# Performance work log

Hardware: AMD Instinct MI355X
Metric: run time of the kernel (lower is better)

Reference implementation:

```python
import jax, jax.numpy as jnp
import numpy as np

EMBED_DIM = 1024
NUM_HEADS = 16
HEAD_DIM = EMBED_DIM // NUM_HEADS
B, S = 2, 2048


def setup_inputs() -> dict:
    key = jax.random.key(0)
    ks = jax.random.split(key, 9)
    scale = 1.0 / np.sqrt(EMBED_DIM)
    return {
        "x": jax.random.normal(ks[0], (B, S, EMBED_DIM), dtype=jnp.float32),
        "Wq": jax.random.normal(ks[1], (EMBED_DIM, EMBED_DIM), dtype=jnp.float32) * scale,
        "bq": jnp.zeros((EMBED_DIM,), dtype=jnp.float32),
        "Wk": jax.random.normal(ks[2], (EMBED_DIM, EMBED_DIM), dtype=jnp.float32) * scale,
        "bk": jnp.zeros((EMBED_DIM,), dtype=jnp.float32),
        "Wv": jax.random.normal(ks[3], (EMBED_DIM, EMBED_DIM), dtype=jnp.float32) * scale,
        "bv": jnp.zeros((EMBED_DIM,), dtype=jnp.float32),
        "Wo": jax.random.normal(ks[4], (EMBED_DIM, EMBED_DIM), dtype=jnp.float32) * scale,
        "bo": jnp.zeros((EMBED_DIM,), dtype=jnp.float32),
    }


def _split_heads(t):
    # [B, S, E] -> [B, H, S, Dh]
    b, s, _ = t.shape
    return t.reshape(b, s, NUM_HEADS, HEAD_DIM).transpose(0, 2, 1, 3)


def reference(x, Wq, bq, Wk, bk, Wv, bv, Wo, bo):
    q = _split_heads(x @ Wq + bq)
    k = _split_heads(x @ Wk + bk)
    v = _split_heads(x @ Wv + bv)
    scale = jnp.sqrt(jnp.asarray(HEAD_DIM, dtype=x.dtype))
    scores = jnp.einsum("bhqd,bhkd->bhqk", q, k) / scale
    attn = jax.nn.softmax(scores, axis=-1)
    out = jnp.einsum("bhqk,bhkd->bhqd", attn, v)  # [B,H,S,Dh]
    out = out.transpose(0, 2, 1, 3).reshape(x.shape[0], x.shape[1], EMBED_DIM)
    return out @ Wo + bo
```

## Files before the change

### kernel.cpp

```cpp
#include <hip/hip_runtime.h>
#include <math.h>
#include <stdint.h>

typedef __bf16 bf16;
typedef __bf16 bf16x4 __attribute__((ext_vector_type(4)));
typedef __bf16 bf16x8 __attribute__((ext_vector_type(8)));
typedef float f32x4 __attribute__((ext_vector_type(4)));

constexpr int E = 1024;
constexpr int S = 2048;
constexpr int H = 16;

__device__ __forceinline__ void gload16(const void* g, void* l) {
  __builtin_amdgcn_global_load_lds(
      (__attribute__((address_space(1))) void*)(uintptr_t)g,
      (__attribute__((address_space(3))) void*)(uint32_t)(uintptr_t)l, 16, 0, 0);
}

__device__ __forceinline__ f32x4 mfma16(bf16x8 a, bf16x8 b, f32x4 c) {
  return __builtin_amdgcn_mfma_f32_16x16x32_bf16(a, b, c, 0, 0, 0);
}

__global__ __launch_bounds__(256) void cast_x(const float* __restrict__ x,
                                              bf16* __restrict__ o) {
  const size_t i = ((size_t)blockIdx.x * 256 + threadIdx.x) * 8;
  const float4 a = *(const float4*)(x + i);
  const float4 b = *(const float4*)(x + i + 4);
  bf16x8 r;
  r[0] = (bf16)a.x; r[1] = (bf16)a.y; r[2] = (bf16)a.z; r[3] = (bf16)a.w;
  r[4] = (bf16)b.x; r[5] = (bf16)b.y; r[6] = (bf16)b.z; r[7] = (bf16)b.w;
  *(bf16x8*)(o + i) = r;
}

__global__ __launch_bounds__(256) void transpose_cast_w(
    const float* __restrict__ W0, const float* __restrict__ W1,
    const float* __restrict__ W2, const float* __restrict__ W3,
    bf16* __restrict__ T0, bf16* __restrict__ T1, bf16* __restrict__ T2,
    bf16* __restrict__ T3) {
  const float* W;
  bf16* T;
  switch (blockIdx.z) {
    case 0: W = W0; T = T0; break;
    case 1: W = W1; T = T1; break;
    case 2: W = W2; T = T2; break;
    default: W = W3; T = T3; break;
  }
  __shared__ float t[64][65];
  const int k0 = blockIdx.y * 64, n0 = blockIdx.x * 64;
  const int tr = threadIdx.x >> 4;
  const int tc = (threadIdx.x & 15) * 4;
#pragma unroll
  for (int u = 0; u < 4; ++u) {
    const float4 v = *(const float4*)(W + (size_t)(k0 + tr + u * 16) * E + n0 + tc);
    t[tr + u * 16][tc + 0] = v.x;
    t[tr + u * 16][tc + 1] = v.y;
    t[tr + u * 16][tc + 2] = v.z;
    t[tr + u * 16][tc + 3] = v.w;
  }
  __syncthreads();
#pragma unroll
  for (int u = 0; u < 4; ++u) {
    const int n = tr + u * 16;
    bf16x4 o;
#pragma unroll
    for (int i = 0; i < 4; ++i) o[i] = (bf16)t[tc + i][n];
    *(bf16x4*)(T + (size_t)(n0 + n) * E + k0 + tc) = o;
  }
}

__global__ __launch_bounds__(256) void gemm_qkv(const bf16* __restrict__ A,
                                                const bf16* __restrict__ Wt,
                                                const float* __restrict__ bq,
                                                const float* __restrict__ bk,
                                                const float* __restrict__ bv,
                                                bf16* __restrict__ qo,
                                                bf16* __restrict__ ko,
                                                bf16* __restrict__ vo) {
  __shared__ __attribute__((aligned(16))) bf16 Asm[128 * 32];
  __shared__ __attribute__((aligned(16))) bf16 Bsm[128 * 32];
  const int z = blockIdx.z;
  const bf16* Bt = Wt + (size_t)z * E * E;
  const float* bias = (z == 0) ? bq : (z == 1) ? bk : bv;
  const int tid = threadIdx.x;
  const int w = tid >> 6, lane = tid & 63, quad = lane >> 4, ln = lane & 15;
  const int bm = blockIdx.y * 128, bn = blockIdx.x * 128;
  const int wr = w >> 1, wc = w & 1;
  const int srow = w * 32 + (lane >> 2);
  const int scol = (lane & 3) * 8;
  const bf16* Ag = A + (size_t)(bm + srow) * E + scol;
  const bf16* Bg = Bt + (size_t)(bn + srow) * E + scol;
  f32x4 acc[4][4] = {};

  for (int k0 = 0; k0 < E; k0 += 32) {
    gload16(Ag + k0, &Asm[(w * 32) * 32]);
    gload16(Ag + k0 + (size_t)16 * E, &Asm[(w * 32 + 16) * 32]);
    gload16(Bg + k0, &Bsm[(w * 32) * 32]);
    gload16(Bg + k0 + (size_t)16 * E, &Bsm[(w * 32 + 16) * 32]);
    __syncthreads();
    bf16x8 af[4], bfr[4];
#pragma unroll
    for (int t = 0; t < 4; ++t) {
      af[t] = *(const bf16x8*)&Asm[(wr * 64 + t * 16 + ln) * 32 + quad * 8];
      bfr[t] = *(const bf16x8*)&Bsm[(wc * 64 + t * 16 + ln) * 32 + quad * 8];
    }
#pragma unroll
    for (int rt = 0; rt < 4; ++rt)
#pragma unroll
      for (int ct = 0; ct < 4; ++ct)
        acc[rt][ct] = mfma16(af[rt], bfr[ct], acc[rt][ct]);
    __syncthreads();
  }

  const float scl = (z == 0) ? 0.125f : 1.0f;
  float bvv[4];
#pragma unroll
  for (int ct = 0; ct < 4; ++ct) bvv[ct] = bias[bn + wc * 64 + ct * 16 + ln];
#pragma unroll
  for (int rt = 0; rt < 4; ++rt) {
    const int row0 = bm + wr * 64 + rt * 16 + quad * 4;
#pragma unroll
    for (int ct = 0; ct < 4; ++ct) {
      const int c = bn + wc * 64 + ct * 16 + ln;
      if (z == 2) {
        bf16x4 p;
#pragma unroll
        for (int r = 0; r < 4; ++r) p[r] = (bf16)(acc[rt][ct][r] + bvv[ct]);
        const int bb = row0 >> 11;
        const int sin = row0 & 2047;
        *(bf16x4*)&vo[((size_t)(bb << 10) + c) * S + sin] = p;
      } else {
        bf16* o = (z == 0) ? qo : ko;
#pragma unroll
        for (int r = 0; r < 4; ++r)
          o[(size_t)(row0 + r) * E + c] = (bf16)((acc[rt][ct][r] + bvv[ct]) * scl);
      }
    }
  }
}

__global__ __launch_bounds__(256) void gemm_wo(const bf16* __restrict__ A,
                                               const bf16* __restrict__ Bt,
                                               const float* __restrict__ bias,
                                               float* __restrict__ C) {
  __shared__ __attribute__((aligned(16))) bf16 Asm[64 * 32];
  __shared__ __attribute__((aligned(16))) bf16 Bsm[128 * 32];
  const int tid = threadIdx.x;
  const int w = tid >> 6, lane = tid & 63, quad = lane >> 4, ln = lane & 15;
  const int bm = blockIdx.y * 64, bn = blockIdx.x * 128;
  const int wr = w >> 1, wc = w & 1;
  const int sr = lane >> 2, sc = (lane & 3) * 8;
  const bf16* Ag = A + (size_t)(bm + w * 16 + sr) * E + sc;
  const bf16* Bg = Bt + (size_t)(bn + w * 32 + sr) * E + sc;
  f32x4 acc[2][4] = {};

  for (int k0 = 0; k0 < E; k0 += 32) {
    gload16(Ag + k0, &Asm[(w * 16) * 32]);
    gload16(Bg + k0, &Bsm[(w * 32) * 32]);
    gload16(Bg + k0 + (size_t)16 * E, &Bsm[(w * 32 + 16) * 32]);
    __syncthreads();
    bf16x8 af[2], bfr[4];
#pragma unroll
    for (int t = 0; t < 2; ++t)
      af[t] = *(const bf16x8*)&Asm[(wr * 32 + t * 16 + ln) * 32 + quad * 8];
#pragma unroll
    for (int t = 0; t < 4; ++t)
      bfr[t] = *(const bf16x8*)&Bsm[(wc * 64 + t * 16 + ln) * 32 + quad * 8];
#pragma unroll
    for (int rt = 0; rt < 2; ++rt)
#pragma unroll
      for (int ct = 0; ct < 4; ++ct)
        acc[rt][ct] = mfma16(af[rt], bfr[ct], acc[rt][ct]);
    __syncthreads();
  }

  float bvv[4];
#pragma unroll
  for (int ct = 0; ct < 4; ++ct) bvv[ct] = bias[bn + wc * 64 + ct * 16 + ln];
#pragma unroll
  for (int rt = 0; rt < 2; ++rt) {
    const int row0 = bm + wr * 32 + rt * 16 + quad * 4;
#pragma unroll
    for (int ct = 0; ct < 4; ++ct) {
      const int c = bn + wc * 64 + ct * 16 + ln;
#pragma unroll
      for (int r = 0; r < 4; ++r)
        C[(size_t)(row0 + r) * E + c] = acc[rt][ct][r] + bvv[ct];
    }
  }
}

__global__ __launch_bounds__(256) void attn_mfma(const bf16* __restrict__ Qg,
                                                 const bf16* __restrict__ Kg,
                                                 const bf16* __restrict__ Vt,
                                                 bf16* __restrict__ Og) {
  __shared__ __attribute__((aligned(16))) bf16 Qs[2][64][32];
  __shared__ __attribute__((aligned(16))) bf16 Ks[2][2][64][32];
  __shared__ __attribute__((aligned(16))) bf16 Vs[2][2][64][32];
  __shared__ __attribute__((aligned(16))) bf16 Pl[4][16][72];
  const int tid = threadIdx.x;
  const int w = tid >> 6, lane = tid & 63, quad = lane >> 4, ln = lane & 15;
  const int q0 = blockIdx.x * 64, h = blockIdx.y, b = blockIdx.z;
  const size_t qkb = ((size_t)b * S) * E + (size_t)h * 64;
  const size_t vtb = ((size_t)b * E + (size_t)h * 64) * S;
  const int sr = lane >> 2, sc = (lane & 3) * 8;

#pragma unroll
  for (int hf = 0; hf < 2; ++hf)
    gload16(Qg + qkb + (size_t)(q0 + w * 16 + sr) * E + hf * 32 + sc,
            &Qs[hf][w * 16][0]);

  const bf16* Kp = Kg + qkb + (size_t)(w * 16 + sr) * E + sc;
  const bf16* Vp = Vt + vtb + (size_t)(w * 16 + sr) * S + sc;

  bf16x8 kr[2], vr[2];
#pragma unroll
  for (int hf = 0; hf < 2; ++hf) {
    kr[hf] = *(const bf16x8*)(Kp + hf * 32);
    vr[hf] = *(const bf16x8*)(Vp + hf * 32);
  }
#pragma unroll
  for (int hf = 0; hf < 2; ++hf) {
    *(bf16x8*)&Ks[0][hf][w * 16 + sr][sc] = kr[hf];
    *(bf16x8*)&Vs[0][hf][w * 16 + sr][sc] = vr[hf];
  }

  float lpart[4] = {};
  f32x4 oacc[4] = {};
  bf16x8 qf[2];
  int cur = 0;

  for (int kt = 0; kt < S; kt += 64) {
    __syncthreads();
    const bool more = (kt + 64 < S);
    if (more) {
#pragma unroll
      for (int hf = 0; hf < 2; ++hf) {
        kr[hf] = *(const bf16x8*)(Kp + (size_t)(kt + 64) * E + hf * 32);
        vr[hf] = *(const bf16x8*)(Vp + (kt + 64) + hf * 32);
      }
    }
    if (kt == 0) {
#pragma unroll
      for (int hf = 0; hf < 2; ++hf)
        qf[hf] = *(const bf16x8*)&Qs[hf][w * 16 + ln][quad * 8];
    }

    f32x4 sc4[4];
#pragma unroll
    for (int ct = 0; ct < 4; ++ct) {
      f32x4 z = {};
      z = mfma16(qf[0], *(const bf16x8*)&Ks[cur][0][ct * 16 + ln][quad * 8], z);
      z = mfma16(qf[1], *(const bf16x8*)&Ks[cur][1][ct * 16 + ln][quad * 8], z);
      sc4[ct] = z;
    }

#pragma unroll
    for (int r = 0; r < 4; ++r) {
#pragma unroll
      for (int ct = 0; ct < 4; ++ct) {
        const float p = __expf(sc4[ct][r]);
        lpart[r] += p;
        Pl[w][quad * 4 + r][ct * 16 + ln] = (bf16)p;
      }
    }
    asm volatile("s_waitcnt lgkmcnt(0)" ::: "memory");
    const bf16x8 pf0 = *(const bf16x8*)&Pl[w][ln][quad * 8];
    const bf16x8 pf1 = *(const bf16x8*)&Pl[w][ln][32 + quad * 8];
#pragma unroll
    for (int ct = 0; ct < 4; ++ct) {
      oacc[ct] = mfma16(pf0, *(const bf16x8*)&Vs[cur][0][ct * 16 + ln][quad * 8],
                        oacc[ct]);
      oacc[ct] = mfma16(pf1, *(const bf16x8*)&Vs[cur][1][ct * 16 + ln][quad * 8],
                        oacc[ct]);
    }

    if (more) {
#pragma unroll
      for (int hf = 0; hf < 2; ++hf) {
        *(bf16x8*)&Ks[cur ^ 1][hf][w * 16 + sr][sc] = kr[hf];
        *(bf16x8*)&Vs[cur ^ 1][hf][w * 16 + sr][sc] = vr[hf];
      }
    }
    cur ^= 1;
  }

#pragma unroll
  for (int r = 0; r < 4; ++r) {
#pragma unroll
    for (int off = 1; off < 16; off <<= 1) lpart[r] += __shfl_xor(lpart[r], off);
  }
  float inv[4];
#pragma unroll
  for (int r = 0; r < 4; ++r) inv[r] = 1.0f / lpart[r];
#pragma unroll
  for (int ct = 0; ct < 4; ++ct) {
#pragma unroll
    for (int r = 0; r < 4; ++r) {
      Og[qkb + (size_t)(q0 + w * 16 + quad * 4 + r) * E + ct * 16 + ln] =
          (bf16)(oacc[ct][r] * inv[r]);
    }
  }
}

extern "C" void kernel_launch(void* const* d_in, const int* in_sizes, int n_in,
                              void* d_out, int out_size, void* d_ws, size_t ws_size,
                              hipStream_t stream) {
  const float* x = (const float*)d_in[0];
  const float* Wq = (const float*)d_in[1];
  const float* bq = (const float*)d_in[2];
  const float* Wk = (const float*)d_in[3];
  const float* bk = (const float*)d_in[4];
  const float* Wv = (const float*)d_in[5];
  const float* bv = (const float*)d_in[6];
  const float* Wo = (const float*)d_in[7];
  const float* bo = (const float*)d_in[8];

  const size_t ME = (size_t)4096 * 1024;
  const size_t WE = (size_t)1024 * 1024;
  bf16* xb = (bf16*)d_ws;
  bf16* wqt = xb + ME;
  bf16* wkt = wqt + WE;
  bf16* wvt = wkt + WE;
  bf16* wot = wvt + WE;
  bf16* qb = wot + WE;
  bf16* kb = qb + ME;
  bf16* vt = kb + ME;
  bf16* ab = vt + ME;

  cast_x<<<2048, 256, 0, stream>>>(x, xb);
  transpose_cast_w<<<dim3(16, 16, 4), 256, 0, stream>>>(Wq, Wk, Wv, Wo, wqt, wkt,
                                                        wvt, wot);
  gemm_qkv<<<dim3(8, 32, 3), 256, 0, stream>>>(xb, wqt, bq, bk, bv, qb, kb, vt);
  attn_mfma<<<dim3(32, 16, 2), 256, 0, stream>>>(qb, kb, vt, ab);
  gemm_wo<<<dim3(8, 64), 256, 0, stream>>>(ab, wot, bo, (float*)d_out);
}
```

Before: 209.6 us.

## Use 32x32 MFMA tiles with 128 queries per attention block

Rewrites the attention kernel to use 32x32x16 bf16 MFMA, with each wave handling 32 query rows and computing transposed scores so softmax outputs map directly to row-per-lane layout. Each block now covers 128 queries, doubling reuse of every K/V tile loaded into shared memory and halving the grid. Q is held in registers, loaded directly from global memory, and the LDS tiles are padded. The trade-off is fewer blocks for the GPU's CUs and higher register pressure from the 16-wide accumulators.

```diff
diff --git a/kernel.cpp b/kernel.cpp
--- a/kernel.cpp
+++ b/kernel.cpp
@@ -6,6 +6,7 @@
 typedef __bf16 bf16x4 __attribute__((ext_vector_type(4)));
 typedef __bf16 bf16x8 __attribute__((ext_vector_type(8)));
 typedef float f32x4 __attribute__((ext_vector_type(4)));
+typedef float f32x16 __attribute__((ext_vector_type(16)));
 
 constexpr int E = 1024;
 constexpr int S = 2048;
@@ -19,6 +20,9 @@
 
 __device__ __forceinline__ f32x4 mfma16(bf16x8 a, bf16x8 b, f32x4 c) {
   return __builtin_amdgcn_mfma_f32_16x16x32_bf16(a, b, c, 0, 0, 0);
+}
+__device__ __forceinline__ f32x16 mfma32(bf16x8 a, bf16x8 b, f32x16 c) {
+  return __builtin_amdgcn_mfma_f32_32x32x16_bf16(a, b, c, 0, 0, 0);
 }
 
 __global__ __launch_bounds__(256) void cast_x(const float* __restrict__ x,
@@ -193,111 +197,113 @@
                                                  const bf16* __restrict__ Kg,
                                                  const bf16* __restrict__ Vt,
                                                  bf16* __restrict__ Og) {
-  __shared__ __attribute__((aligned(16))) bf16 Qs[2][64][32];
-  __shared__ __attribute__((aligned(16))) bf16 Ks[2][2][64][32];
-  __shared__ __attribute__((aligned(16))) bf16 Vs[2][2][64][32];
-  __shared__ __attribute__((aligned(16))) bf16 Pl[4][16][72];
+  __shared__ __attribute__((aligned(16))) bf16 Ks[2][64][72];
+  __shared__ __attribute__((aligned(16))) bf16 Vs[2][64][72];
+  __shared__ __attribute__((aligned(16))) bf16 Pl[4][32][72];
   const int tid = threadIdx.x;
-  const int w = tid >> 6, lane = tid & 63, quad = lane >> 4, ln = lane & 15;
-  const int q0 = blockIdx.x * 64, h = blockIdx.y, b = blockIdx.z;
+  const int w = tid >> 6, lane = tid & 63, ln = lane & 31, hf = lane >> 5;
+  const int q0 = blockIdx.x * 128, h = blockIdx.y, b = blockIdx.z;
   const size_t qkb = ((size_t)b * S) * E + (size_t)h * 64;
   const size_t vtb = ((size_t)b * E + (size_t)h * 64) * S;
-  const int sr = lane >> 2, sc = (lane & 3) * 8;
-
-#pragma unroll
-  for (int hf = 0; hf < 2; ++hf)
-    gload16(Qg + qkb + (size_t)(q0 + w * 16 + sr) * E + hf * 32 + sc,
-            &Qs[hf][w * 16][0]);
-
-  const bf16* Kp = Kg + qkb + (size_t)(w * 16 + sr) * E + sc;
-  const bf16* Vp = Vt + vtb + (size_t)(w * 16 + sr) * S + sc;
+  const int sr = tid >> 2;
+  const int sc = (tid & 3) * 16;
+
+  bf16x8 qf[4];
+  {
+    const bf16* qrow = Qg + qkb + (size_t)(q0 + w * 32 + ln) * E + hf * 8;
+#pragma unroll
+    for (int c = 0; c < 4; ++c) qf[c] = *(const bf16x8*)(qrow + 16 * c);
+  }
+
+  const bf16* Kp = Kg + qkb + (size_t)sr * E + sc;
+  const bf16* Vp = Vt + vtb + (size_t)sr * S + sc;
 
   bf16x8 kr[2], vr[2];
-#pragma unroll
-  for (int hf = 0; hf < 2; ++hf) {
-    kr[hf] = *(const bf16x8*)(Kp + hf * 32);
-    vr[hf] = *(const bf16x8*)(Vp + hf * 32);
-  }
-#pragma unroll
-  for (int hf = 0; hf < 2; ++hf) {
-    *(bf16x8*)&Ks[0][hf][w * 16 + sr][sc] = kr[hf];
-    *(bf16x8*)&Vs[0][hf][w * 16 + sr][sc] = vr[hf];
-  }
-
-  float lpart[4] = {};
-  f32x4 oacc[4] = {};
-  bf16x8 qf[2];
+  kr[0] = *(const bf16x8*)(Kp);
+  kr[1] = *(const bf16x8*)(Kp + 8);
+  vr[0] = *(const bf16x8*)(Vp);
+  vr[1] = *(const bf16x8*)(Vp + 8);
+  *(bf16x8*)&Ks[0][sr][sc] = kr[0];
+  *(bf16x8*)&Ks[0][sr][sc + 8] = kr[1];
+  *(bf16x8*)&Vs[0][sr][sc] = vr[0];
+  *(bf16x8*)&Vs[0][sr][sc + 8] = vr[1];
+
+  float lpart = 0.f;
+  f32x16 oacc[2] = {};
   int cur = 0;
 
   for (int kt = 0; kt < S; kt += 64) {
     __syncthreads();
     const bool more = (kt + 64 < S);
     if (more) {
-#pragma unroll
-      for (int hf = 0; hf < 2; ++hf) {
-        kr[hf] = *(const bf16x8*)(Kp + (size_t)(kt + 64) * E + hf * 32);
-        vr[hf] = *(const bf16x8*)(Vp + (kt + 64) + hf * 32);
+      kr[0] = *(const bf16x8*)(Kp + (size_t)(kt + 64) * E);
+      kr[1] = *(const bf16x8*)(Kp + (size_t)(kt + 64) * E + 8);
+      vr[0] = *(const bf16x8*)(Vp + (kt + 64));
+      vr[1] = *(const bf16x8*)(Vp + (kt + 64) + 8);
+    }
+
+    f32x16 st[2] = {};
+#pragma unroll
+    for (int mt = 0; mt < 2; ++mt) {
+#pragma unroll
+      for (int c = 0; c < 4; ++c) {
+        const bf16x8 ka =
+            *(const bf16x8*)&Ks[cur][mt * 32 + ln][c * 16 + hf * 8];
+        st[mt] = mfma32(ka, qf[c], st[mt]);
       }
     }
-    if (kt == 0) {
-#pragma unroll
-      for (int hf = 0; hf < 2; ++hf)
-        qf[hf] = *(const bf16x8*)&Qs[hf][w * 16 + ln][quad * 8];
-    }
-
-    f32x4 sc4[4];
-#pragma unroll
-    for (int ct = 0; ct < 4; ++ct) {
-      f32x4 z = {};
-      z = mfma16(qf[0], *(const bf16x8*)&Ks[cur][0][ct * 16 + ln][quad * 8], z);
-      z = mfma16(qf[1], *(const bf16x8*)&Ks[cur][1][ct * 16 + ln][quad * 8], z);
-      sc4[ct] = z;
-    }
-
-#pragma unroll
-    for (int r = 0; r < 4; ++r) {
-#pragma unroll
-      for (int ct = 0; ct < 4; ++ct) {
-        const float p = __expf(sc4[ct][r]);
-        lpart[r] += p;
-        Pl[w][quad * 4 + r][ct * 16 + ln] = (bf16)p;
+
+#pragma unroll
+    for (int mt = 0; mt < 2; ++mt) {
+#pragma unroll
+      for (int g = 0; g < 4; ++g) {
+        bf16x4 pk;
+#pragma unroll
+        for (int j = 0; j < 4; ++j) {
+          const float p = __expf(st[mt][g * 4 + j]);
+          lpart += p;
+          pk[j] = (bf16)p;
+        }
+        *(bf16x4*)&Pl[w][ln][mt * 32 + g * 8 + hf * 4] = pk;
       }
     }
     asm volatile("s_waitcnt lgkmcnt(0)" ::: "memory");
-    const bf16x8 pf0 = *(const bf16x8*)&Pl[w][ln][quad * 8];
-    const bf16x8 pf1 = *(const bf16x8*)&Pl[w][ln][32 + quad * 8];
-#pragma unroll
-    for (int ct = 0; ct < 4; ++ct) {
-      oacc[ct] = mfma16(pf0, *(const bf16x8*)&Vs[cur][0][ct * 16 + ln][quad * 8],
-                        oacc[ct]);
-      oacc[ct] = mfma16(pf1, *(const bf16x8*)&Vs[cur][1][ct * 16 + ln][quad * 8],
-                        oacc[ct]);
+
+    bf16x8 pb[4];
+#pragma unroll
+    for (int c = 0; c < 4; ++c)
+      pb[c] = *(const bf16x8*)&Pl[w][ln][c * 16 + hf * 8];
+#pragma unroll
+    for (int mt = 0; mt < 2; ++mt) {
+#pragma unroll
+      for (int c = 0; c < 4; ++c) {
+        const bf16x8 va =
+            *(const bf16x8*)&Vs[cur][mt * 32 + ln][c * 16 + hf * 8];
+        oacc[mt] = mfma32(va, pb[c], oacc[mt]);
+      }
     }
 
     if (more) {
-#pragma unroll
-      for (int hf = 0; hf < 2; ++hf) {
-        *(bf16x8*)&Ks[cur ^ 1][hf][w * 16 + sr][sc] = kr[hf];
-        *(bf16x8*)&Vs[cur ^ 1][hf][w * 16 + sr][sc] = vr[hf];
-      }
+      *(bf16x8*)&Ks[cur ^ 1][sr][sc] = kr[0];
+      *(bf16x8*)&Ks[cur ^ 1][sr][sc + 8] = kr[1];
+      *(bf16x8*)&Vs[cur ^ 1][sr][sc] = vr[0];
+      *(bf16x8*)&Vs[cur ^ 1][sr][sc + 8] = vr[1];
     }
     cur ^= 1;
   }
 
-#pragma unroll
-  for (int r = 0; r < 4; ++r) {
-#pragma unroll
-    for (int off = 1; off < 16; off <<= 1) lpart[r] += __shfl_xor(lpart[r], off);
-  }
-  float inv[4];
-#pragma unroll
-  for (int r = 0; r < 4; ++r) inv[r] = 1.0f / lpart[r];
-#pragma unroll
-  for (int ct = 0; ct < 4; ++ct) {
-#pragma unroll
-    for (int r = 0; r < 4; ++r) {
-      Og[qkb + (size_t)(q0 + w * 16 + quad * 4 + r) * E + ct * 16 + ln] =
-          (bf16)(oacc[ct][r] * inv[r]);
+  lpart += __shfl_xor(lpart, 32);
+  const float inv = 1.0f / lpart;
+
+  bf16* orow = Og + qkb + (size_t)(q0 + w * 32 + ln) * E;
+#pragma unroll
+  for (int mt = 0; mt < 2; ++mt) {
+#pragma unroll
+    for (int g = 0; g < 4; ++g) {
+      bf16x4 o;
+#pragma unroll
+      for (int j = 0; j < 4; ++j) o[j] = (bf16)(oacc[mt][g * 4 + j] * inv);
+      *(bf16x4*)&orow[mt * 32 + g * 8 + hf * 4] = o;
     }
   }
 }
@@ -331,6 +337,6 @@
   transpose_cast_w<<<dim3(16, 16, 4), 256, 0, stream>>>(Wq, Wk, Wv, Wo, wqt, wkt,
                                                         wvt, wot);
   gemm_qkv<<<dim3(8, 32, 3), 256, 0, stream>>>(xb, wqt, bq, bk, bv, qb, kb, vt);
-  attn_mfma<<<dim3(32, 16, 2), 256, 0, stream>>>(qb, kb, vt, ab);
+  attn_mfma<<<dim3(16, 16, 2), 256, 0, stream>>>(qb, kb, vt, ab);
   gemm_wo<<<dim3(8, 64), 256, 0, stream>>>(ab, wot, bo, (float*)d_out);
 }
```

Result: faster. 202.6 us (-3.3%).
